# Kernel optimization log

Hardware: AMD Instinct MI355X
Metric: run time of the kernel (lower is better)

Reference implementation:

```python
import jax, jax.numpy as jnp
import numpy as np

IN_CH, OUT_CH, K, UP = 512, 256, 3, 2
WSCALE = float(1.0 / np.sqrt(K * K * IN_CH))  # use_wscale gain / sqrt(fan_in), lr_mul=1
ACT_GAIN = float(np.sqrt(2.0))                # lrelu def_gain
CLAMP = 256.0                                  # conv_clamp * runtime_gain(=1)
FIR_PAD = 1                                    # px0+pxt = px1+pxt = 1 (derived in forward)

def _fir_filter():
    # upfirdn2d.setup_filter([1,3,3,1]): outer product then normalize to sum 1
    f1 = jnp.array([1.0, 3.0, 3.0, 1.0], jnp.float32)
    f2 = jnp.outer(f1, f1)
    return f2 / jnp.sum(f2)  # (4,4), sums to 1

def setup_inputs() -> dict:
    key = jax.random.key(0)
    k1, k2 = jax.random.split(key)
    return {
        "x": jax.random.normal(k1, (16, IN_CH, 64, 64), jnp.float32),
        "weight": jax.random.normal(k2, (OUT_CH, IN_CH, K, K), jnp.float32),
        "bias": jnp.zeros((OUT_CH,), jnp.float32),
    }

def _forward(x, weight, bias):
    w = weight * WSCALE  # runtime weight scaling
    # torch conv_transpose2d(x, w.transpose(0,1), stride=UP, padding=0)
    # == lhs-dilated correlation with spatially flipped kernel, pad K-1 each side
    k = w[:, :, ::-1, ::-1]
    y = jax.lax.conv_general_dilated(
        x, k, window_strides=(1, 1),
        padding=((K - 1, K - 1), (K - 1, K - 1)),
        lhs_dilation=(UP, UP),
        dimension_numbers=('NCHW', 'OIHW', 'NCHW'))  # (N, OUT_CH, 129, 129)
    # upfirdn2d(up=1, padding=(1,1,1,1), gain=UP**2):
    # pad, then depthwise conv with flipped filter scaled by gain**(ndim/2)=UP*UP
    f = _fir_filter() * (UP * UP)
    y = jnp.pad(y, ((0, 0), (0, 0), (FIR_PAD, FIR_PAD), (FIR_PAD, FIR_PAD)))
    fk = jnp.broadcast_to(f[::-1, ::-1][None, None], (OUT_CH, 1, 4, 4))
    y = jax.lax.conv_general_dilated(
        y, fk, (1, 1), 'VALID',
        feature_group_count=OUT_CH,
        dimension_numbers=('NCHW', 'OIHW', 'NCHW'))  # (N, OUT_CH, 128, 128)
    # bias_act: bias add, leaky_relu(0.2), gain sqrt(2), clamp +-256
    y = y + bias[None, :, None, None]
    y = jnp.where(y >= 0, y, 0.2 * y) * ACT_GAIN
    return jnp.clip(y, -CLAMP, CLAMP)

def reference(x, weight, bias):
    return _forward(x, weight, bias)
```

## Files before the change

### kernel.cpp

```cpp
#include <hip/hip_runtime.h>
#include <hip/hip_bf16.h>

#define NIMG 16
#define IN_CH 512
#define OUT_CH 256
#define HIN 64
#define HOUT 128
#define HP 66

#define WSCALE 0.014731391f
#define ACT_GAIN 1.41421356237f
#define CLAMP_V 256.0f

typedef __attribute__((ext_vector_type(8))) short bf16x8;
typedef __attribute__((ext_vector_type(4))) float f32x4;

__device__ __constant__ float c_G[2][3][3] = {
    {{0.00f, 0.25f, 0.75f}, {0.75f, 0.75f, 0.25f}, {0.25f, 0.00f, 0.00f}},
    {{0.00f, 0.00f, 0.25f}, {0.25f, 0.75f, 0.75f}, {0.75f, 0.25f, 0.00f}}
};

#define XBF_BYTES ((size_t)NIMG * HP * HP * IN_CH * 2)
#define EBF_BYTES ((size_t)9 * 1024 * IN_CH * 2)
#define WS_NEED (XBF_BYTES + EBF_BYTES)

__global__ __launch_bounds__(256) void xpose_kernel(const float* __restrict__ x,
                                                    __hip_bfloat16* __restrict__ xbf) {
    const int n = blockIdx.z;
    const int hp = blockIdx.y;
    const int c0 = blockIdx.x << 6;
    const int tid = threadIdx.x;
    const size_t obase = ((size_t)n * HP + hp) * HP;

    if (hp == 0 || hp == HP - 1) {
        for (int idx = tid; idx < HP * 64; idx += 256) {
            int wp = idx >> 6, c = idx & 63;
            xbf[(obase + wp) * IN_CH + c0 + c] = __float2bfloat16(0.f);
        }
        return;
    }
    __shared__ float tile[64][65];
    {
        int cc = tid >> 6, w = tid & 63;
        for (int cb = 0; cb < 64; cb += 4)
            tile[cb + cc][w] =
                x[(((size_t)n * IN_CH + c0 + cb + cc) * HIN + (hp - 1)) * HIN + w];
    }
    __syncthreads();
    {
        int c = tid & 63, wg = tid >> 6;
        for (int wb = 0; wb < 64; wb += 4) {
            int w2 = wb + wg;
            xbf[(obase + (w2 + 1)) * IN_CH + c0 + c] = __float2bfloat16(tile[c][w2]);
        }
        if (tid < 128) {
            int which = tid >> 6, c2 = tid & 63;
            xbf[(obase + (which ? (HP - 1) : 0)) * IN_CH + c0 + c2] = __float2bfloat16(0.f);
        }
    }
}

__global__ __launch_bounds__(256) void build_ebf_kernel(const float* __restrict__ w,
                                                        __hip_bfloat16* __restrict__ ebf) {
    int gid = blockIdx.x * 256 + threadIdx.x;
    if (gid >= OUT_CH * IN_CH) return;
    int oc = gid >> 9, c = gid & 511;
    float wm[3][3];
    const float* wp = w + (size_t)gid * 9;
#pragma unroll
    for (int a = 0; a < 3; ++a)
#pragma unroll
        for (int b = 0; b < 3; ++b) wm[a][b] = wp[a * 3 + b] * WSCALE;
#pragma unroll
    for (int i = 0; i < 3; ++i)
#pragma unroll
        for (int j = 0; j < 3; ++j)
#pragma unroll
            for (int pu = 0; pu < 2; ++pu)
#pragma unroll
                for (int pv = 0; pv < 2; ++pv) {
                    float s = 0.f;
#pragma unroll
                    for (int a = 0; a < 3; ++a)
#pragma unroll
                        for (int b = 0; b < 3; ++b)
                            s += wm[a][b] * c_G[pu][i][a] * c_G[pv][j][b];
                    ebf[((size_t)(i * 3 + j) * 1024 + oc * 4 + pu * 2 + pv) * IN_CH + c] =
                        __float2bfloat16(s);
                }
}

__global__ __launch_bounds__(512, 2) void mfma_conv8_kernel(
    const __hip_bfloat16* __restrict__ xbf, const __hip_bfloat16* __restrict__ ebf,
    const float* __restrict__ bias, float* __restrict__ out) {
    __shared__ __align__(16) char lds[131072];

    const int tid = threadIdx.x;
    const int lane = tid & 63;
    const int wid = tid >> 6;
    const int wy = wid >> 2;
    const int wx = wid & 3;
    const int lm = lane & 15, lk = lane >> 4;

    const int bid = blockIdx.x;
    const int wkid = ((bid & 7) << 7) + (bid >> 3);
    const int mtile = wkid >> 2;
    const int ntile = wkid & 3;
    const int n = mtile >> 4;
    const int sub = mtile & 15;
    const int qh0 = (sub >> 2) << 4;
    const int qw0 = (sub & 3) << 4;
    const int n0 = ntile << 8;

    const int qc_s = lane >> 2;
    const int src_slot = (((lane & 3) ^ ((lane >> 3) & 3)) << 3);

    f32x4 acc[8][4];
#pragma unroll
    for (int mi = 0; mi < 8; ++mi)
#pragma unroll
        for (int ni = 0; ni < 4; ++ni) acc[mi][ni] = (f32x4)(0.f);

    auto stage = [&](int s) {
        const int tt2 = s >> 2;
        const int part = s & 3;
        const int mat = part & 1;
        const int kh = part >> 1;
        const int tap = tt2 >> 3;
        const int chan = ((tt2 & 7) << 6) + (kh << 5) + src_slot;
        char* dst = lds + ((((tt2 & 1) << 2) | (mat << 1) | kh) << 14) + (wid << 10);
        if (mat == 0) {
            const int fi = (tap * 171) >> 9;
            const int fj = tap - fi * 3;
            const int wp = qw0 + fj + qc_s;
#pragma unroll
            for (int c = 0; c < 2; ++c) {
                const int hp = qh0 + fi + (c << 3) + wid;
                const __hip_bfloat16* src =
                    xbf + (((size_t)n * HP + hp) * HP + wp) * IN_CH + chan;
                __builtin_amdgcn_global_load_lds(
                    (const __attribute__((address_space(1))) unsigned int*)src,
                    (__attribute__((address_space(3))) unsigned int*)(dst + (c << 13)),
                    16, 0, 0);
            }
        } else {
#pragma unroll
            for (int c = 0; c < 2; ++c) {
                const int r = (c << 7) + (wid << 4) + qc_s;
                const __hip_bfloat16* src =
                    ebf + ((size_t)tap * 1024 + n0 + r) * IN_CH + chan;
                __builtin_amdgcn_global_load_lds(
                    (const __attribute__((address_space(1))) unsigned int*)src,
                    (__attribute__((address_space(3))) unsigned int*)(dst + (c << 13)),
                    16, 0, 0);
            }
        }
    };

#pragma unroll
    for (int s = 0; s < 6; ++s) stage(s);
    asm volatile("s_waitcnt vmcnt(4)" ::: "memory");
    __builtin_amdgcn_s_barrier();

    const int rsw = (lm >> 1) & 3;
#pragma unroll 1
    for (int tt = 0; tt < 72; ++tt) {
        const int par = (tt & 1) << 2;
        bf16x8 bfr[4];
#pragma unroll
        for (int p = 0; p < 4; ++p) {
            const int kh = p >> 1, mh = p & 1;
            const char* aslot = lds + ((par | kh) << 14);
            const char* bslot = lds + ((par | 2 | kh) << 14);
            bf16x8 af[4];
#pragma unroll
            for (int mi = 0; mi < 4; ++mi) {
                const int r = (wy << 7) + (mh << 6) + (mi << 4) + lm;
                af[mi] = *(const bf16x8*)(aslot + r * 64 + ((lk ^ rsw) << 4));
            }
            if (mh == 0) {
#pragma unroll
                for (int ni = 0; ni < 4; ++ni) {
                    const int r = (wx << 6) + (ni << 4) + lm;
                    bfr[ni] = *(const bf16x8*)(bslot + r * 64 + ((lk ^ rsw) << 4));
                }
            }
            const int s = tt * 4 + p + 6;
            if (s < 288) stage(s);
            __builtin_amdgcn_s_barrier();
            asm volatile("s_waitcnt lgkmcnt(0)" ::: "memory");
            __builtin_amdgcn_s_setprio(1);
#pragma unroll
            for (int mi = 0; mi < 4; ++mi)
#pragma unroll
                for (int ni = 0; ni < 4; ++ni)
                    acc[mh * 4 + mi][ni] = __builtin_amdgcn_mfma_f32_16x16x32_bf16(
                        af[mi], bfr[ni], acc[mh * 4 + mi][ni], 0, 0, 0);
            __builtin_amdgcn_s_setprio(0);
            if (p == 3) {
                if (tt < 70)
                    asm volatile("s_waitcnt vmcnt(4)" ::: "memory");
                else
                    asm volatile("s_waitcnt vmcnt(0)" ::: "memory");
            }
            __builtin_amdgcn_s_barrier();
        }
    }

    float bv[4];
#pragma unroll
    for (int ni = 0; ni < 4; ++ni)
        bv[ni] = bias[(n0 + (wx << 6) + (ni << 4) + lm) >> 2];
#pragma unroll
    for (int mi8 = 0; mi8 < 8; ++mi8) {
#pragma unroll
        for (int v = 0; v < 4; ++v) {
            const int row = (wy << 7) + (mi8 << 4) + (lk << 2) + v;
            const int qr = row >> 4, qc = row & 15;
            const int hb = 2 * (qh0 + qr), wb = 2 * (qw0 + qc);
#pragma unroll
            for (int ni = 0; ni < 4; ++ni) {
                const int nn = n0 + (wx << 6) + (ni << 4) + lm;
                const int oc = nn >> 2, pu = (nn >> 1) & 1, pv = nn & 1;
                float val = acc[mi8][ni][v] + bv[ni];
                val = (val >= 0.f ? val : 0.2f * val) * ACT_GAIN;
                val = fminf(fmaxf(val, -CLAMP_V), CLAMP_V);
                out[(((size_t)n * OUT_CH + oc) * HOUT + (hb + pu)) * HOUT + (wb + pv)] = val;
            }
        }
    }
}

__global__ void build_e_kernel(const float* __restrict__ w, float* __restrict__ e_ws) {
    int gid = blockIdx.x * blockDim.x + threadIdx.x;
    if (gid >= OUT_CH * IN_CH) return;
    float wm[3][3];
    const float* wp = w + (size_t)gid * 9;
#pragma unroll
    for (int a = 0; a < 3; ++a)
#pragma unroll
        for (int b = 0; b < 3; ++b) wm[a][b] = wp[a * 3 + b] * WSCALE;
    float* op = e_ws + (size_t)gid * 36;
#pragma unroll
    for (int i = 0; i < 3; ++i)
#pragma unroll
        for (int j = 0; j < 3; ++j)
#pragma unroll
            for (int pu = 0; pu < 2; ++pu)
#pragma unroll
                for (int pv = 0; pv < 2; ++pv) {
                    float s = 0.f;
#pragma unroll
                    for (int a = 0; a < 3; ++a)
#pragma unroll
                        for (int b = 0; b < 3; ++b)
                            s += wm[a][b] * c_G[pu][i][a] * c_G[pv][j][b];
                    op[(i * 3 + j) * 4 + pu * 2 + pv] = s;
                }
}

#define OGB 8
#define CB 8
#define QT 16
__global__ __launch_bounds__(256) void fused_conv_kernel(
    const float* __restrict__ x, const float* __restrict__ e_ws,
    const float* __restrict__ bias, float* __restrict__ out) {
    __shared__ float sX[CB][18][19];
    __shared__ float4 sE[OGB * CB * 9];
    const int tid = threadIdx.x;
    const int o2 = tid >> 7;
    const int qy = (tid >> 3) & 15;
    const int qxp = tid & 7;
    const int tileIdx = blockIdx.x;
    const int hq0 = (tileIdx >> 2) * QT;
    const int wq0 = (tileIdx & 3) * QT;
    const int o0 = blockIdx.y * OGB;
    const int n = blockIdx.z;
    float4 acc[2][4];
#pragma unroll
    for (int q = 0; q < 2; ++q)
#pragma unroll
        for (int oo = 0; oo < 4; ++oo) acc[q][oo] = make_float4(0.f, 0.f, 0.f, 0.f);
    for (int c0 = 0; c0 < IN_CH; c0 += CB) {
        for (int idx = tid; idx < CB * 18 * 18; idx += 256) {
            int cc = idx / 324;
            int rem = idx - cc * 324;
            int r = rem / 18;
            int col = rem - r * 18;
            int h = hq0 - 1 + r;
            int ww = wq0 - 1 + col;
            float v = 0.f;
            if (h >= 0 && h < HIN && ww >= 0 && ww < HIN)
                v = x[(((size_t)n * IN_CH + (c0 + cc)) * HIN + h) * HIN + ww];
            sX[cc][r][col] = v;
        }
        {
            float* sEf = (float*)sE;
            for (int idx = tid; idx < OGB * CB * 36; idx += 256) {
                int ol = idx / (CB * 36);
                int rem = idx - ol * (CB * 36);
                sEf[ol * (CB * 36) + rem] =
                    e_ws[((size_t)(o0 + ol) * IN_CH + c0) * 36 + rem];
            }
        }
        __syncthreads();
#pragma unroll 1
        for (int cc = 0; cc < CB; ++cc) {
#pragma unroll
            for (int i = 0; i < 3; ++i) {
#pragma unroll
                for (int j = 0; j < 3; ++j) {
                    float xv0 = sX[cc][qy + i][2 * qxp + j];
                    float xv1 = sX[cc][qy + i][2 * qxp + 1 + j];
#pragma unroll
                    for (int oo = 0; oo < 4; ++oo) {
                        float4 e = sE[((o2 * 4 + oo) * CB + cc) * 9 + i * 3 + j];
                        acc[0][oo].x += xv0 * e.x; acc[0][oo].y += xv0 * e.y;
                        acc[0][oo].z += xv0 * e.z; acc[0][oo].w += xv0 * e.w;
                        acc[1][oo].x += xv1 * e.x; acc[1][oo].y += xv1 * e.y;
                        acc[1][oo].z += xv1 * e.z; acc[1][oo].w += xv1 * e.w;
                    }
                }
            }
        }
        __syncthreads();
    }
#pragma unroll
    for (int q = 0; q < 2; ++q) {
        int qx = 2 * qxp + q;
        int u0 = 2 * (hq0 + qy);
        int v0 = 2 * (wq0 + qx);
#pragma unroll
        for (int oo = 0; oo < 4; ++oo) {
            int o = o0 + o2 * 4 + oo;
            float b = bias[o];
            float vals[4] = {acc[q][oo].x, acc[q][oo].y, acc[q][oo].z, acc[q][oo].w};
#pragma unroll
            for (int p = 0; p < 4; ++p) {
                int pu = p >> 1, pv = p & 1;
                float v = vals[p] + b;
                v = (v >= 0.f ? v : 0.2f * v) * ACT_GAIN;
                v = fminf(fmaxf(v, -CLAMP_V), CLAMP_V);
                out[(((size_t)n * OUT_CH + o) * HOUT + (u0 + pu)) * HOUT + (v0 + pv)] = v;
            }
        }
    }
}

extern "C" void kernel_launch(void* const* d_in, const int* in_sizes, int n_in,
                              void* d_out, int out_size, void* d_ws, size_t ws_size,
                              hipStream_t stream) {
    const float* x = (const float*)d_in[0];
    const float* w = (const float*)d_in[1];
    const float* bias = (const float*)d_in[2];
    float* out = (float*)d_out;

    if (ws_size >= WS_NEED) {
        __hip_bfloat16* xbf = (__hip_bfloat16*)d_ws;
        __hip_bfloat16* ebf = (__hip_bfloat16*)((char*)d_ws + XBF_BYTES);
        xpose_kernel<<<dim3(8, HP, NIMG), 256, 0, stream>>>(x, xbf);
        build_ebf_kernel<<<(OUT_CH * IN_CH + 255) / 256, 256, 0, stream>>>(w, ebf);
        mfma_conv8_kernel<<<dim3(1024), 512, 0, stream>>>(xbf, ebf, bias, out);
    } else {
        float* e_ws = (float*)d_ws;
        build_e_kernel<<<(OUT_CH * IN_CH + 255) / 256, 256, 0, stream>>>(w, e_ws);
        dim3 grid(16, OUT_CH / OGB, NIMG);
        fused_conv_kernel<<<grid, 256, 0, stream>>>(x, e_ws, bias, out);
    }
}
```

Baseline: 685.8 us.

## Software-pipeline LDS fragment loads one phase ahead of MFMA with register double buffering

Restructures the main loop so that A/B fragments for the next MFMA phase are read from LDS into alternate register buffers while the current phase's MFMAs run. It also replaces the per-phase lgkmcnt(0) with partial waits and sched_barriers, and adjusts the vmcnt waits and stage scheduling. The goal is to hide LDS read latency behind matrix math and drop one barrier per phase. In exchange it uses more VGPRs, which may hurt occupancy at 2 blocks/CU, and it relies on hand-counted waitcnt values being correct.

```diff
diff --git a/kernel.cpp b/kernel.cpp
--- a/kernel.cpp
+++ b/kernel.cpp
@@ -89,6 +89,14 @@
                         __float2bfloat16(s);
                 }
 }
+
+#define MFMA16(AF, BF, MH)                                                        \
+    do {                                                                          \
+        _Pragma("unroll") for (int mi = 0; mi < 4; ++mi)                          \
+            _Pragma("unroll") for (int ni = 0; ni < 4; ++ni)                      \
+                acc[(MH)*4 + mi][ni] = __builtin_amdgcn_mfma_f32_16x16x32_bf16(   \
+                    (AF)[mi], (BF)[ni], acc[(MH)*4 + mi][ni], 0, 0, 0);           \
+    } while (0)
 
 __global__ __launch_bounds__(512, 2) void mfma_conv8_kernel(
     const __hip_bfloat16* __restrict__ xbf, const __hip_bfloat16* __restrict__ ebf,
@@ -157,54 +165,90 @@
         }
     };
 
+    const int rsw = (lm >> 1) & 3;
+
+    auto pfA = [&](bf16x8* dst, int par_, int kh, int mh) {
+        const char* aslot = lds + (((par_ << 2) | kh) << 14);
+        const int rb = (wy << 7) + (mh << 6) + lm;
+#pragma unroll
+        for (int mi = 0; mi < 4; ++mi)
+            dst[mi] = *(const bf16x8*)(aslot + (rb + (mi << 4)) * 64 + ((lk ^ rsw) << 4));
+    };
+    auto pfB = [&](bf16x8* dst, int par_, int kh) {
+        const char* bslot = lds + (((par_ << 2) | 2 | kh) << 14);
+        const int rb = (wx << 6) + lm;
+#pragma unroll
+        for (int ni = 0; ni < 4; ++ni)
+            dst[ni] = *(const bf16x8*)(bslot + (rb + (ni << 4)) * 64 + ((lk ^ rsw) << 4));
+    };
+
 #pragma unroll
     for (int s = 0; s < 6; ++s) stage(s);
-    asm volatile("s_waitcnt vmcnt(4)" ::: "memory");
+    asm volatile("s_waitcnt vmcnt(8)" ::: "memory");
     __builtin_amdgcn_s_barrier();
-
-    const int rsw = (lm >> 1) & 3;
+    __builtin_amdgcn_sched_barrier(0);
+
+    bf16x8 afE[4], afO[4], b0[4], b1[4];
+    pfA(afE, 0, 0, 0);
+    pfB(b0, 0, 0);
+
 #pragma unroll 1
     for (int tt = 0; tt < 72; ++tt) {
-        const int par = (tt & 1) << 2;
-        bf16x8 bfr[4];
-#pragma unroll
-        for (int p = 0; p < 4; ++p) {
-            const int kh = p >> 1, mh = p & 1;
-            const char* aslot = lds + ((par | kh) << 14);
-            const char* bslot = lds + ((par | 2 | kh) << 14);
-            bf16x8 af[4];
-#pragma unroll
-            for (int mi = 0; mi < 4; ++mi) {
-                const int r = (wy << 7) + (mh << 6) + (mi << 4) + lm;
-                af[mi] = *(const bf16x8*)(aslot + r * 64 + ((lk ^ rsw) << 4));
-            }
-            if (mh == 0) {
-#pragma unroll
-                for (int ni = 0; ni < 4; ++ni) {
-                    const int r = (wx << 6) + (ni << 4) + lm;
-                    bfr[ni] = *(const bf16x8*)(bslot + r * 64 + ((lk ^ rsw) << 4));
-                }
-            }
-            const int s = tt * 4 + p + 6;
-            if (s < 288) stage(s);
-            __builtin_amdgcn_s_barrier();
+        const int par = tt & 1, npar = par ^ 1;
+        pfA(afO, par, 0, 1);
+        if (tt <= 70) stage(4 * tt + 6);
+        asm volatile("s_waitcnt lgkmcnt(4)" ::: "memory");
+        __builtin_amdgcn_sched_barrier(0);
+        __builtin_amdgcn_s_setprio(1);
+        MFMA16(afE, b0, 0);
+        __builtin_amdgcn_s_setprio(0);
+        if (tt < 69)
+            asm volatile("s_waitcnt vmcnt(6)" ::: "memory");
+        else
+            asm volatile("s_waitcnt vmcnt(0)" ::: "memory");
+        __builtin_amdgcn_s_barrier();
+        __builtin_amdgcn_sched_barrier(0);
+
+        pfA(afE, par, 1, 0);
+        pfB(b1, par, 1);
+        if (tt <= 70) stage(4 * tt + 7);
+        asm volatile("s_waitcnt lgkmcnt(8)" ::: "memory");
+        __builtin_amdgcn_sched_barrier(0);
+        __builtin_amdgcn_s_setprio(1);
+        MFMA16(afO, b0, 1);
+        __builtin_amdgcn_s_setprio(0);
+        __builtin_amdgcn_s_barrier();
+        __builtin_amdgcn_sched_barrier(0);
+
+        pfA(afO, par, 1, 1);
+        if (tt <= 69) stage(4 * tt + 8);
+        asm volatile("s_waitcnt lgkmcnt(4)" ::: "memory");
+        __builtin_amdgcn_sched_barrier(0);
+        __builtin_amdgcn_s_setprio(1);
+        MFMA16(afE, b1, 0);
+        __builtin_amdgcn_s_setprio(0);
+        if (tt < 69)
+            asm volatile("s_waitcnt vmcnt(6)" ::: "memory");
+        else
+            asm volatile("s_waitcnt vmcnt(0)" ::: "memory");
+        __builtin_amdgcn_s_barrier();
+        __builtin_amdgcn_sched_barrier(0);
+
+        if (tt < 71) {
+            pfA(afE, npar, 0, 0);
+            pfB(b0, npar, 0);
+        }
+        if (tt <= 69) stage(4 * tt + 9);
+        if (tt < 71)
+            asm volatile("s_waitcnt lgkmcnt(8)" ::: "memory");
+        else
             asm volatile("s_waitcnt lgkmcnt(0)" ::: "memory");
-            __builtin_amdgcn_s_setprio(1);
-#pragma unroll
-            for (int mi = 0; mi < 4; ++mi)
-#pragma unroll
-                for (int ni = 0; ni < 4; ++ni)
-                    acc[mh * 4 + mi][ni] = __builtin_amdgcn_mfma_f32_16x16x32_bf16(
-                        af[mi], bfr[ni], acc[mh * 4 + mi][ni], 0, 0, 0);
-            __builtin_amdgcn_s_setprio(0);
-            if (p == 3) {
-                if (tt < 70)
-                    asm volatile("s_waitcnt vmcnt(4)" ::: "memory");
-                else
-                    asm volatile("s_waitcnt vmcnt(0)" ::: "memory");
-            }
-            __builtin_amdgcn_s_barrier();
-        }
+        __builtin_amdgcn_sched_barrier(0);
+        __builtin_amdgcn_s_setprio(1);
+        MFMA16(afO, b1, 1);
+        __builtin_amdgcn_s_setprio(0);
+        __builtin_amdgcn_s_barrier();
+        __builtin_amdgcn_sched_barrier(0);
     }
 
     float bv[4];
```

Result: no change. 673.2 us (-1.8%).

## Software-pipeline LDS fragment loads with MFMA and hand-schedule async global-to-LDS staging

Applied to the files above, without the earlier changes.

Replaces the main K loop with a hand-unrolled two-iteration macro. The next A/B fragments are read from LDS while the current MFMA block runs, using partial lgkmcnt/vmcnt waits and sched_barriers in place of full lgkmcnt(0) waits. Staging addresses become incrementally advanced pointers with precomputed wrap offsets instead of being recomputed per stage. This raises register pressure from double-buffered fragments and depends on fragile hand-tuned wait counts and pointer jumps being correct.

```diff
diff --git a/kernel.cpp b/kernel.cpp
--- a/kernel.cpp
+++ b/kernel.cpp
@@ -89,6 +89,102 @@
                         __float2bfloat16(s);
                 }
 }
+
+#define MFMA16(AF, BF, MH)                                                        \
+    do {                                                                          \
+        _Pragma("unroll") for (int mi = 0; mi < 4; ++mi)                          \
+            _Pragma("unroll") for (int ni = 0; ni < 4; ++ni)                      \
+                acc[(MH)*4 + mi][ni] = __builtin_amdgcn_mfma_f32_16x16x32_bf16(   \
+                    (AF)[mi], (BF)[ni], acc[(MH)*4 + mi][ni], 0, 0, 0);           \
+    } while (0)
+
+#define CJA 270336
+#define CJB 65536
+#define DAK1(PAR) (((((PAR) ^ 1) << 2) | 1) << 14)
+#define DBK1(PAR) (((((PAR) ^ 1) << 2) | 3) << 14)
+#define DAK0(PAR) ((((PAR) << 2) | 0) << 14)
+#define DBK0(PAR) ((((PAR) << 2) | 2) << 14)
+
+#define GLL(SRC, DSTOFF)                                                          \
+    __builtin_amdgcn_global_load_lds(                                             \
+        (const __attribute__((address_space(1))) unsigned int*)(SRC),             \
+        (__attribute__((address_space(3))) unsigned int*)(ldsW + (DSTOFF)), 16, 0, 0)
+
+#define TILE_ITER(PAR, TT, SP01, SP23, VMS, LGK3, LAST)                           \
+    {                                                                             \
+        const char* aP = (PAR) ? aBaseO : aBaseE;                                 \
+        const char* bP = (PAR) ? bBaseO : bBaseE;                                 \
+                 \
+        afO[0] = *(const bf16x8*)(aP + 4096);                                     \
+        afO[1] = *(const bf16x8*)(aP + 4096 + 1024);                              \
+        afO[2] = *(const bf16x8*)(aP + 4096 + 2048);                              \
+        afO[3] = *(const bf16x8*)(aP + 4096 + 3072);                              \
+        if (SP01) { GLL(pAK1, DAK1(PAR)); GLL(pAK1 + CJA, DAK1(PAR) + 8192); }    \
+        pAK1 += ((TT) == 22 || (TT) == 46) ? 32320 : 64;                          \
+        asm volatile("s_waitcnt lgkmcnt(4)" ::: "memory");                        \
+        __builtin_amdgcn_sched_barrier(0);                                        \
+        __builtin_amdgcn_s_setprio(1);                                            \
+        MFMA16(afE, b0, 0);                                                       \
+        __builtin_amdgcn_s_setprio(0);                                            \
+        asm volatile("s_waitcnt " VMS ::: "memory");                              \
+        __builtin_amdgcn_s_barrier();                                             \
+        __builtin_amdgcn_sched_barrier(0);                                        \
+              \
+        afE[0] = *(const bf16x8*)(aP + 16384);                                    \
+        afE[1] = *(const bf16x8*)(aP + 16384 + 1024);                             \
+        afE[2] = *(const bf16x8*)(aP + 16384 + 2048);                             \
+        afE[3] = *(const bf16x8*)(aP + 16384 + 3072);                             \
+        b1[0] = *(const bf16x8*)(bP + 16384);                                     \
+        b1[1] = *(const bf16x8*)(bP + 16384 + 1024);                              \
+        b1[2] = *(const bf16x8*)(bP + 16384 + 2048);                              \
+        b1[3] = *(const bf16x8*)(bP + 16384 + 3072);                              \
+        if (SP01) { GLL(pBK1, DBK1(PAR)); GLL(pBK1 + CJB, DBK1(PAR) + 8192); }    \
+        pBK1 += (((TT) & 7) == 6) ? 523840 : 64;                                  \
+        asm volatile("s_waitcnt lgkmcnt(8)" ::: "memory");                        \
+        __builtin_amdgcn_sched_barrier(0);                                        \
+        __builtin_amdgcn_s_setprio(1);                                            \
+        MFMA16(afO, b0, 1);                                                       \
+        __builtin_amdgcn_s_setprio(0);                                            \
+        __builtin_amdgcn_s_barrier();                                             \
+        __builtin_amdgcn_sched_barrier(0);                                        \
+                      \
+        afO[0] = *(const bf16x8*)(aP + 20480);                                    \
+        afO[1] = *(const bf16x8*)(aP + 20480 + 1024);                             \
+        afO[2] = *(const bf16x8*)(aP + 20480 + 2048);                             \
+        afO[3] = *(const bf16x8*)(aP + 20480 + 3072);                             \
+        if (SP23) { GLL(pAK0, DAK0(PAR)); GLL(pAK0 + CJA, DAK0(PAR) + 8192); }    \
+        pAK0 += ((TT) == 21 || (TT) == 45) ? 32320 : 64;                          \
+        asm volatile("s_waitcnt lgkmcnt(4)" ::: "memory");                        \
+        __builtin_amdgcn_sched_barrier(0);                                        \
+        __builtin_amdgcn_s_setprio(1);                                            \
+        MFMA16(afE, b1, 0);                                                       \
+        __builtin_amdgcn_s_setprio(0);                                            \
+        asm volatile("s_waitcnt " VMS ::: "memory");                              \
+        __builtin_amdgcn_s_barrier();                                             \
+        __builtin_amdgcn_sched_barrier(0);                                        \
+           \
+        if (!(LAST)) {                                                            \
+            const char* aN = (PAR) ? aBaseE : aBaseO;                             \
+            const char* bN = (PAR) ? bBaseE : bBaseO;                             \
+            afE[0] = *(const bf16x8*)(aN);                                        \
+            afE[1] = *(const bf16x8*)(aN + 1024);                                 \
+            afE[2] = *(const bf16x8*)(aN + 2048);                                 \
+            afE[3] = *(const bf16x8*)(aN + 3072);                                 \
+            b0[0] = *(const bf16x8*)(bN);                                         \
+            b0[1] = *(const bf16x8*)(bN + 1024);                                  \
+            b0[2] = *(const bf16x8*)(bN + 2048);                                  \
+            b0[3] = *(const bf16x8*)(bN + 3072);                                  \
+        }                                                                         \
+        if (SP23) { GLL(pBK0, DBK0(PAR)); GLL(pBK0 + CJB, DBK0(PAR) + 8192); }    \
+        pBK0 += (((TT) & 7) == 5) ? 523840 : 64;                                  \
+        asm volatile("s_waitcnt " LGK3 ::: "memory");                             \
+        __builtin_amdgcn_sched_barrier(0);                                        \
+        __builtin_amdgcn_s_setprio(1);                                            \
+        MFMA16(afO, b1, 1);                                                       \
+        __builtin_amdgcn_s_setprio(0);                                            \
+        __builtin_amdgcn_s_barrier();                                             \
+        __builtin_amdgcn_sched_barrier(0);                                        \
+    }
 
 __global__ __launch_bounds__(512, 2) void mfma_conv8_kernel(
     const __hip_bfloat16* __restrict__ xbf, const __hip_bfloat16* __restrict__ ebf,
@@ -120,6 +216,8 @@
     for (int mi = 0; mi < 8; ++mi)
 #pragma unroll
         for (int ni = 0; ni < 4; ++ni) acc[mi][ni] = (f32x4)(0.f);
+
+    char* ldsW = lds + (wid << 10);
 
     auto stage = [&](int s) {
         const int tt2 = s >> 2;
@@ -157,55 +255,45 @@
         }
     };
 
+    const int rsw = (lm >> 1) & 3;
+    const char* aBaseE = lds + ((wy << 7) + lm) * 64 + ((lk ^ rsw) << 4);
+    const char* aBaseO = aBaseE + 65536;
+    const char* bBaseE = lds + 32768 + ((wx << 6) + lm) * 64 + ((lk ^ rsw) << 4);
+    const char* bBaseO = bBaseE + 65536;
+
+    const __hip_bfloat16* pixA =
+        xbf + (((size_t)n * HP + qh0 + wid) * HP + qw0 + qc_s) * IN_CH;
+    const __hip_bfloat16* pAK1 = pixA + 96 + src_slot;
+    const __hip_bfloat16* pAK0 = pixA + 128 + src_slot;
+    const __hip_bfloat16* rowB = ebf + ((size_t)n0 + (wid << 4) + qc_s) * IN_CH;
+    const __hip_bfloat16* pBK1 = rowB + 96 + src_slot;
+    const __hip_bfloat16* pBK0 = rowB + 128 + src_slot;
+
 #pragma unroll
     for (int s = 0; s < 6; ++s) stage(s);
-    asm volatile("s_waitcnt vmcnt(4)" ::: "memory");
+    asm volatile("s_waitcnt vmcnt(8)" ::: "memory");
     __builtin_amdgcn_s_barrier();
-
-    const int rsw = (lm >> 1) & 3;
+    __builtin_amdgcn_sched_barrier(0);
+
+    bf16x8 afE[4], afO[4], b0[4], b1[4];
+    afE[0] = *(const bf16x8*)(aBaseE);
+    afE[1] = *(const bf16x8*)(aBaseE + 1024);
+    afE[2] = *(const bf16x8*)(aBaseE + 2048);
+    afE[3] = *(const bf16x8*)(aBaseE + 3072);
+    b0[0] = *(const bf16x8*)(bBaseE);
+    b0[1] = *(const bf16x8*)(bBaseE + 1024);
+    b0[2] = *(const bf16x8*)(bBaseE + 2048);
+    b0[3] = *(const bf16x8*)(bBaseE + 3072);
+
 #pragma unroll 1
-    for (int tt = 0; tt < 72; ++tt) {
-        const int par = (tt & 1) << 2;
-        bf16x8 bfr[4];
-#pragma unroll
-        for (int p = 0; p < 4; ++p) {
-            const int kh = p >> 1, mh = p & 1;
-            const char* aslot = lds + ((par | kh) << 14);
-            const char* bslot = lds + ((par | 2 | kh) << 14);
-            bf16x8 af[4];
-#pragma unroll
-            for (int mi = 0; mi < 4; ++mi) {
-                const int r = (wy << 7) + (mh << 6) + (mi << 4) + lm;
-                af[mi] = *(const bf16x8*)(aslot + r * 64 + ((lk ^ rsw) << 4));
-            }
-            if (mh == 0) {
-#pragma unroll
-                for (int ni = 0; ni < 4; ++ni) {
-                    const int r = (wx << 6) + (ni << 4) + lm;
-                    bfr[ni] = *(const bf16x8*)(bslot + r * 64 + ((lk ^ rsw) << 4));
-                }
-            }
-            const int s = tt * 4 + p + 6;
-            if (s < 288) stage(s);
-            __builtin_amdgcn_s_barrier();
-            asm volatile("s_waitcnt lgkmcnt(0)" ::: "memory");
-            __builtin_amdgcn_s_setprio(1);
-#pragma unroll
-            for (int mi = 0; mi < 4; ++mi)
-#pragma unroll
-                for (int ni = 0; ni < 4; ++ni)
-                    acc[mh * 4 + mi][ni] = __builtin_amdgcn_mfma_f32_16x16x32_bf16(
-                        af[mi], bfr[ni], acc[mh * 4 + mi][ni], 0, 0, 0);
-            __builtin_amdgcn_s_setprio(0);
-            if (p == 3) {
-                if (tt < 70)
-                    asm volatile("s_waitcnt vmcnt(4)" ::: "memory");
-                else
-                    asm volatile("s_waitcnt vmcnt(0)" ::: "memory");
-            }
-            __builtin_amdgcn_s_barrier();
-        }
-    }
+    for (int tt = 0; tt < 68; tt += 2) {
+        TILE_ITER(0, tt, 1, 1, "vmcnt(6)", "lgkmcnt(8)", 0);
+        TILE_ITER(1, tt + 1, 1, 1, "vmcnt(6)", "lgkmcnt(8)", 0);
+    }
+    TILE_ITER(0, 68, 1, 1, "vmcnt(6)", "lgkmcnt(8)", 0);
+    TILE_ITER(1, 69, 1, 1, "vmcnt(0)", "lgkmcnt(8)", 0);
+    TILE_ITER(0, 70, 1, 0, "vmcnt(0)", "lgkmcnt(8)", 0);
+    TILE_ITER(1, 71, 0, 0, "vmcnt(0)", "lgkmcnt(0)", 1);
 
     float bv[4];
 #pragma unroll
```

Result: faster. 619.3 us (-9.7%).
